# Performance work log

Measured on AMD Instinct MI355X. Metric: run time of the kernel, lower is better.

Reference implementation:

```python
import jax, jax.numpy as jnp
import numpy as np

CONF_THRES = 0.1
IOU_THRES = 0.6
MAX_DET = 300
MAX_WH = 4096.0  # class offset for non-agnostic NMS
NEG_SLOPE = 0.01  # nn.LeakyReLU default


def xywh2xyxy(p):
    xy, wh = p[..., :2], p[..., 2:4]
    return jnp.concatenate([xy - wh / 2, xy + wh / 2], axis=-1)


def pairwise_iou(a, b):
    area_a = (a[:, 2] - a[:, 0]) * (a[:, 3] - a[:, 1])
    area_b = (b[:, 2] - b[:, 0]) * (b[:, 3] - b[:, 1])
    lt = jnp.maximum(a[:, None, :2], b[None, :, :2])
    rb = jnp.minimum(a[:, None, 2:], b[None, :, 2:])
    wh = jnp.clip(rb - lt, 0.0)
    inter = wh[..., 0] * wh[..., 1]
    return inter / (area_a[:, None] + area_b[None, :] - inter + 1e-7)


def nms_single(pred):  # pred: [N, 5+nc]
    boxes = xywh2xyxy(pred[:, :4])
    scores = pred[:, 5:] * pred[:, 4:5]  # obj * cls
    conf = jnp.max(scores, axis=1)
    cls = jnp.argmax(scores, axis=1)
    conf = jnp.where(conf > CONF_THRES, conf, 0.0)
    topv, topi = jax.lax.top_k(conf, MAX_DET)
    b = boxes[topi]                      # [K,4]
    c = cls[topi]
    valid = topv > CONF_THRES
    bo = b + (c.astype(b.dtype) * MAX_WH)[:, None]  # class-offset boxes
    iou = pairwise_iou(bo, bo)           # [K,K]
    idx = jnp.arange(MAX_DET)
    def body(i, keep):
        sup = keep[i] & (iou[i] > IOU_THRES) & (idx > i)
        return keep & ~sup
    keep = jax.lax.fori_loop(0, MAX_DET, body, valid)
    return b, keep


def bilinear_sample(feat, y, x):  # feat [C,H,W], y/x [K,P] -> [C,K,P]
    C, H, W = feat.shape
    y = jnp.clip(y, 0.0, H - 1.0)
    x = jnp.clip(x, 0.0, W - 1.0)
    y0 = jnp.floor(y).astype(jnp.int32)
    x0 = jnp.floor(x).astype(jnp.int32)
    y1 = jnp.minimum(y0 + 1, H - 1)
    x1 = jnp.minimum(x0 + 1, W - 1)
    ly = y - y0
    lx = x - x0
    return (feat[:, y0, x0] * ((1 - ly) * (1 - lx))
            + feat[:, y0, x1] * ((1 - ly) * lx)
            + feat[:, y1, x0] * (ly * (1 - lx))
            + feat[:, y1, x1] * (ly * lx))


def roi_align_1x1(feat, boxes, scale):  # feat [C,H,W], boxes [K,4] xyxy (input-px)
    b = boxes * scale
    w = jnp.maximum(b[:, 2] - b[:, 0], 1.0)
    h = jnp.maximum(b[:, 3] - b[:, 1], 1.0)
    off = jnp.array([0.5, 1.5], dtype=boxes.dtype)
    xs = b[:, 0:1] + off[None, :] * (w[:, None] / 2.0)  # [K,2]
    ys = b[:, 1:2] + off[None, :] * (h[:, None] / 2.0)
    yy = ys[:, jnp.array([0, 0, 1, 1])]  # [K,4] 2x2 grid
    xx = xs[:, jnp.array([0, 1, 0, 1])]
    v = bilinear_sample(feat, yy, xx)    # [C,K,4]
    return jnp.mean(v, axis=2).T         # [K,C]


def rescale_boxes(bbox, hw, hw0):  # scale_coords + normalize by orig shape
    gain = jnp.minimum(hw[0] / hw0[0], hw[1] / hw0[1])
    pad_x = (hw[1] - hw0[1] * gain) / 2.0
    pad_y = (hw[0] - hw0[0] * gain) / 2.0
    x1 = jnp.clip((bbox[:, 0] - pad_x) / gain, 0.0, hw0[1])
    y1 = jnp.clip((bbox[:, 1] - pad_y) / gain, 0.0, hw0[0])
    x2 = jnp.clip((bbox[:, 2] - pad_x) / gain, 0.0, hw0[1])
    y2 = jnp.clip((bbox[:, 3] - pad_y) / gain, 0.0, hw0[0])
    # divide by shapes[i][0] indexed [w,h,w,h]
    return jnp.stack([x1 / hw0[1], y1 / hw0[0], x2 / hw0[1], y2 / hw0[0]], axis=1)


def setup_inputs() -> dict:
    key = jax.random.key(0)
    ks = jax.random.split(key, 10)
    B, N, NC = 8, 25500, 80
    xy = jax.random.uniform(ks[0], (B, N, 2), minval=0.0, maxval=640.0)
    wh = jax.random.uniform(ks[1], (B, N, 2), minval=8.0, maxval=160.0)
    obj = jax.random.uniform(ks[2], (B, N, 1))
    cls = jax.random.uniform(ks[3], (B, N, NC))
    preds = jnp.concatenate([xy, wh, obj, cls], axis=-1)
    feat1 = jax.random.normal(ks[4], (B, 128, 80, 80), dtype=jnp.float32)
    feat2 = jax.random.normal(ks[5], (B, 256, 40, 40), dtype=jnp.float32)
    feat3 = jax.random.normal(ks[6], (B, 512, 20, 20), dtype=jnp.float32)
    feat4 = jax.random.normal(ks[7], (B, 1024, 10, 10), dtype=jnp.float32)
    orig_hw = jnp.tile(jnp.array([[720.0, 1280.0]], dtype=jnp.float32), (B, 1))
    W1 = jax.random.normal(ks[8], (1920, 256), dtype=jnp.float32) * 0.02
    b1 = jnp.zeros((256,), dtype=jnp.float32)
    W2 = jax.random.normal(ks[9], (256, 256), dtype=jnp.float32) * 0.02
    b2 = jnp.zeros((256,), dtype=jnp.float32)
    return {"preds": preds, "feat1": feat1, "feat2": feat2, "feat3": feat3,
            "feat4": feat4, "orig_hw": orig_hw, "W1": W1, "b1": b1,
            "W2": W2, "b2": b2}


def reference(preds, feat1, feat2, feat3, feat4, orig_hw, W1, b1, W2, b2):
    preds = jax.lax.stop_gradient(preds)  # out.detach() in the original
    hw = jnp.array(feat1.shape[-2:], dtype=preds.dtype) * 8.0  # network input h,w
    boxes, keep = jax.vmap(nms_single)(preds)  # [B,K,4], [B,K]
    f1 = jax.vmap(lambda f, b: roi_align_1x1(f, b, 1.0 / 8))(feat1, boxes)
    f2 = jax.vmap(lambda f, b: roi_align_1x1(f, b, 1.0 / 16))(feat2, boxes)
    f3 = jax.vmap(lambda f, b: roi_align_1x1(f, b, 1.0 / 32))(feat3, boxes)
    f4 = jax.vmap(lambda f, b: roi_align_1x1(f, b, 1.0 / 64))(feat4, boxes)
    f = jnp.concatenate([f1, f2, f3, f4], axis=-1)  # [B,K,1920]
    h = jax.nn.leaky_relu(f @ W1 + b1, NEG_SLOPE)
    h = jax.nn.leaky_relu(h @ W2 + b2, NEG_SLOPE)   # [B,K,256]
    bb = jax.vmap(lambda b, s: rescale_boxes(b, hw, s))(boxes, orig_hw)
    out = jnp.concatenate([bb, h], axis=-1)  # [B,K,260]
    return out * keep[..., None].astype(out.dtype)
```

## Files before the change

### kernel.cpp

```cpp
#include <hip/hip_runtime.h>
#include <hip/hip_bf16.h>
#include <cstdint>
#include <cstddef>

#define NBATCH 8
#define NANCH 25500
#define MAXDET 300
#define NBINS 2048
#define SCAT_BLKS 64

typedef __bf16 bf16x8 __attribute__((ext_vector_type(8)));
typedef float floatx4 __attribute__((ext_vector_type(4)));
typedef unsigned long long ull;

__device__ __forceinline__ int conf_bin(float v) {
  unsigned bits = __float_as_uint(v);
  int bin = (int)((bits - 0x3D800000u) >> 14);
  return bin > (NBINS - 1) ? (NBINS - 1) : bin;
}

#define CONF_TILE 64
__global__ __launch_bounds__(256) void conf_kernel(const float* __restrict__ preds,
                                                   float* __restrict__ conf,
                                                   int* __restrict__ cls,
                                                   int* __restrict__ ghist, int total) {
  __shared__ float s[CONF_TILE * 85];
  int base = blockIdx.x * CONF_TILE;
  int nA = total - base; if (nA > CONF_TILE) nA = CONF_TILE;
  int n4 = (nA * 85) >> 2;
  const float4* g4 = (const float4*)(preds + (size_t)base * 85);
  float4* s4 = (float4*)s;
  for (int i = threadIdx.x; i < n4; i += 256) s4[i] = g4[i];
  __syncthreads();
  int lane16 = threadIdx.x & 15;
  int sub = threadIdx.x >> 4;
  #pragma unroll
  for (int r = 0; r < 4; ++r) {
    int a = r * 16 + sub;
    if (a < nA) {
      const float* row = s + a * 85;
      float obj = row[4];
      float best = -1.0f; int bc = 0;
      #pragma unroll
      for (int j = 0; j < 5; ++j) {
        int c = lane16 * 5 + j;
        float v = row[5 + c] * obj;
        if (v > best) { best = v; bc = c; }
      }
      #pragma unroll
      for (int m = 1; m < 16; m <<= 1) {
        float ov = __shfl_xor(best, m, 64);
        int   oc = __shfl_xor(bc,   m, 64);
        if (ov > best || (ov == best && oc < bc)) { best = ov; bc = oc; }
      }
      if (lane16 == 0) {
        int idx = base + a;
        bool pass = best > 0.1f;
        conf[idx] = pass ? best : 0.0f;
        cls[idx] = bc;
        if (pass) {
          int b = idx / NANCH;
          atomicAdd(&ghist[b * NBINS + conf_bin(best)], 1);
        }
      }
    }
  }
}

struct TransArgs {
  const float* src[6];
  __hip_bfloat16* dst[6];
  int C[6], HW[6], tx[6], tpb[6], start[6];
};

__global__ __launch_bounds__(256) void trans_scatter_kernel(TransArgs a,
                                                            const float* __restrict__ conf,
                                                            const float* __restrict__ preds,
                                                            const int* __restrict__ clsg,
                                                            const int* __restrict__ ghist,
                                                            int* __restrict__ gcnt,
                                                            float* __restrict__ gV,
                                                            int* __restrict__ gI,
                                                            float4* __restrict__ gBox) {
  #pragma clang fp contract(off)
  __shared__ __align__(16) char smem[8448];
  int bid = blockIdx.x;
  int t = threadIdx.y * 32 + threadIdx.x;

  if (bid < SCAT_BLKS) {
    int b = bid >> 3, seg = bid & 7;
    int* s_suf = (int*)smem;
    int* shv   = (int*)(smem + 8192);
    int r[8], suf[8], rs[8];
    int w = t >> 6, lane = t & 63;
    if (t == 0) shv[0] = NBINS;
    {
      #pragma unroll
      for (int k = 0; k < 8; ++k)
        r[k] = ghist[b * NBINS + (w * 8 + k) * 64 + lane];
      int bsum = 0;
      #pragma unroll
      for (int k = 0; k < 8; ++k) {
        int s = r[k];
        #pragma unroll
        for (int d = 1; d < 64; d <<= 1) {
          int o = __shfl_down(s, d, 64);
          if (lane + d < 64) s += o;
        }
        suf[k] = s - r[k];
        rs[k] = __shfl(s, 0, 64);
        bsum += rs[k];
      }
      if (lane == 0) shv[4 + w] = bsum;
    }
    __syncthreads();
    {
      int p1 = shv[5], p2 = shv[6], p3 = shv[7];
      int total = shv[4] + p1 + p2 + p3;
      int target = total < 300 ? total : 300;
      int RS = (w == 0) ? (p1 + p2 + p3) : (w == 1) ? (p2 + p3) : (w == 2) ? p3 : 0;
      int run = RS;
      #pragma unroll
      for (int k = 7; k >= 0; --k) {
        int Sx = run + suf[k] + r[k];
        int Sx1 = Sx - r[k];
        int bin = (w * 8 + k) * 64 + lane;
        s_suf[bin] = Sx1;
        if (total > 0 && Sx >= target && Sx1 < target) shv[0] = bin;
        run += rs[k];
      }
    }
    __syncthreads();
    int T = shv[0];
    const int N4 = NANCH >> 2;
    int i0 = (N4 * seg) >> 3, i1 = (N4 * (seg + 1)) >> 3;
    const float4* cf4 = (const float4*)(conf + (size_t)b * NANCH);
    for (int i = i0 + t; i < i1; i += 256) {
      float4 v4 = cf4[i];
      int ib = i * 4;
      float vv[4] = {v4.x, v4.y, v4.z, v4.w};
      #pragma unroll
      for (int q = 0; q < 4; ++q) {
        float v = vv[q];
        if (v > 0.1f) {
          int bin = conf_bin(v);
          if (bin >= T) {
            int slot = s_suf[bin] + atomicAdd(&gcnt[b * NBINS + bin], 1);
            int idx = ib + q;
            const float* p = preds + ((size_t)b * NANCH + idx) * 85;
            float cx = p[0], cy = p[1], wq = p[2], hq = p[3];
            float hw2 = wq * 0.5f, hh2 = hq * 0.5f;
            float x1 = cx - hw2, y1 = cy - hh2, x2 = cx + hw2, y2 = cy + hh2;
            int c = clsg[(size_t)b * NANCH + idx];
            size_t g = (size_t)b * NANCH + slot;
            gV[g] = v;
            gI[g] = idx | (c << 20);
            gBox[g] = make_float4(x1, y1, x2, y2);
          }
        }
      }
    }
    return;
  }

  {
    float (*tile)[33] = (float(*)[33])smem;
    int bid2 = bid - SCAT_BLKS;
    int s = 0;
    #pragma unroll
    for (int i = 1; i < 6; ++i) if (bid2 >= a.start[i]) s = i;
    int local = bid2 - a.start[s];
    int C = a.C[s], HW = a.HW[s], tx0 = a.tx[s], tpb = a.tpb[s];
    int b = local / tpb;
    int rem = local - b * tpb;
    int p0 = (rem % tx0) * 32;
    int c0 = (rem / tx0) * 32;
    const float* inb = a.src[s] + (size_t)b * C * HW;
    __hip_bfloat16* outb = a.dst[s] + (size_t)b * C * HW;
    int tx = threadIdx.x, ty = threadIdx.y;
    #pragma unroll
    for (int k = 0; k < 32; k += 8) {
      int c = c0 + ty + k, p = p0 + tx;
      if (c < C && p < HW) tile[ty + k][tx] = inb[(size_t)c * HW + p];
    }
    __syncthreads();
    #pragma unroll
    for (int k = 0; k < 32; k += 8) {
      int p = p0 + ty + k, c = c0 + tx;
      if (p < HW && c < C) outb[(size_t)p * C + c] = __float2bfloat16(tile[tx][ty + k]);
    }
  }
}

__global__ __launch_bounds__(1024) void nms_kernel(const float* __restrict__ gV,
                                                   const int* __restrict__ gI,
                                                   const float4* __restrict__ gBox,
                                                   const int* __restrict__ ghist,
                                                   float* __restrict__ boxesWs, int* __restrict__ keepWs,
                                                   const float* __restrict__ orig_hw,
                                                   float* __restrict__ out) {
  #pragma clang fp contract(off)
  __shared__ __align__(16) char smem[30208];
  int*    s_h  = (int*)smem;
  float4* bo4  = (float4*)(smem + 8192);
  float (*bxx)[4] = (float(*)[4])(smem + 12992);
  ull   (*mask)[5] = (ull(*)[5])(smem + 17792);
  ull* keepw = (ull*)(smem + 29792);
  ull* nzrow = (ull*)(smem + 29832);
  int* shv   = (int*)(smem + 29872);
  int b = blockIdx.x;
  int t = threadIdx.x;

  if (t < 300) {
    bo4[t] = make_float4(0.0f, 0.0f, 0.0f, 0.0f);
    bxx[t][0] = 0.0f; bxx[t][1] = 0.0f; bxx[t][2] = 0.0f; bxx[t][3] = 0.0f;
  }
  if (t < 5) nzrow[t] = 0ULL;
  if (t == 0) { shv[0] = NBINS; shv[2] = 0; }
  {
    int r[8], suf[8], rs[8];
    int w = t >> 6, lane = t & 63;
    if (t < 256) {
      #pragma unroll
      for (int k = 0; k < 8; ++k)
        r[k] = ghist[b * NBINS + (w * 8 + k) * 64 + lane];
      int bsum = 0;
      #pragma unroll
      for (int k = 0; k < 8; ++k) {
        int s = r[k];
        #pragma unroll
        for (int d = 1; d < 64; d <<= 1) {
          int o = __shfl_down(s, d, 64);
          if (lane + d < 64) s += o;
        }
        suf[k] = s - r[k];
        rs[k] = __shfl(s, 0, 64);
        bsum += rs[k];
      }
      if (lane == 0) shv[4 + w] = bsum;
    }
    __syncthreads();
    if (t < 256) {
      int p1 = shv[5], p2 = shv[6], p3 = shv[7];
      int total = shv[4] + p1 + p2 + p3;
      int target = total < 300 ? total : 300;
      int RS = (w == 0) ? (p1 + p2 + p3) : (w == 1) ? (p2 + p3) : (w == 2) ? p3 : 0;
      int run = RS;
      #pragma unroll
      for (int k = 7; k >= 0; --k) {
        int Sx = run + suf[k] + r[k];
        int Sx1 = Sx - r[k];
        int bin = (w * 8 + k) * 64 + lane;
        s_h[bin] = Sx;
        if (total > 0 && Sx >= target && Sx1 < target) { shv[0] = bin; shv[2] = Sx; }
        run += rs[k];
      }
      if (t == 0) shv[1] = total;
    }
  }
  __syncthreads();
  int total = shv[1];
  int Kslots = shv[2];
  int nvalid = total < 300 ? total : 300;

  if (t >= nvalid && t < 300) {
    size_t bi = ((size_t)(b * 300 + t)) * 4;
    boxesWs[bi + 0] = 0.0f; boxesWs[bi + 1] = 0.0f;
    boxesWs[bi + 2] = 0.0f; boxesWs[bi + 3] = 0.0f;
  }
  if (t < 5) {
    int n = nvalid - t * 64;
    keepw[t] = (n <= 0) ? 0ULL : (n >= 64 ? ~0ULL : ((1ULL << n) - 1ULL));
  }

  {
    const float* vb = gV + (size_t)b * NANCH;
    const int*   ib2 = gI + (size_t)b * NANCH;
    for (int sIdx = t; sIdx < Kslots; sIdx += 1024) {
      float v = vb[sIdx];
      unsigned code = (unsigned)ib2[sIdx];
      int id = (int)(code & 0xFFFFFu);
      int bin = conf_bin(v);
      int lo = (bin + 1 < NBINS) ? s_h[bin + 1] : 0;
      int hi = s_h[bin];
      int rank = lo;
      for (int j = lo; j < hi; ++j) {
        float vj = vb[j];
        int ij = ib2[j] & 0xFFFFF;
        int gt = vj > v;
        int eq = (vj == v) & (ij < id);
        rank += gt | eq;
      }
      if (rank < 300) {
        float4 bx = gBox[(size_t)b * NANCH + sIdx];
        bxx[rank][0] = bx.x; bxx[rank][1] = bx.y; bxx[rank][2] = bx.z; bxx[rank][3] = bx.w;
        size_t bi = ((size_t)(b * 300 + rank)) * 4;
        boxesWs[bi + 0] = bx.x; boxesWs[bi + 1] = bx.y;
        boxesWs[bi + 2] = bx.z; boxesWs[bi + 3] = bx.w;
        int c = (int)(code >> 20);
        float off = (float)c * 4096.0f;
        float4 ob; ob.x = bx.x + off; ob.y = bx.y + off; ob.z = bx.z + off; ob.w = bx.w + off;
        bo4[rank] = ob;
      }
    }
  }
  __syncthreads();

  {
    int wv2 = t >> 6, ln = t & 63;
    if (wv2 < 10) {
      int w2 = wv2 >> 1, half = wv2 & 1;
      int j = w2 * 64 + ln;
      int jc = j < 300 ? j : 0;
      float4 jb = bo4[jc];
      float ja = (jb.z - jb.x) * (jb.w - jb.y);
      bool jv = j < 300;
      int iend = w2 * 64 + 64; if (iend > 300) iend = 300;
      int i0 = half * 150, i1 = i0 + 150; if (i1 > iend) i1 = iend;
      #pragma unroll 4
      for (int i = i0; i < i1; ++i) {
        float4 ib = bo4[i];
        float ai = (ib.z - ib.x) * (ib.w - ib.y);
        float ltx = fmaxf(ib.x, jb.x);
        float lty = fmaxf(ib.y, jb.y);
        float rbx = fminf(ib.z, jb.z);
        float rby = fminf(ib.w, jb.w);
        float wx = fmaxf(rbx - ltx, 0.0f);
        float wy = fmaxf(rby - lty, 0.0f);
        float inter = wx * wy;
        float iou = inter / (ai + ja - inter + 1e-7f);
        ull bal = __ballot(jv && (j > i) && (iou > 0.6f));
        if (ln == 0) {
          mask[i][w2] = bal;
          if (bal) atomicOr(&nzrow[i >> 6], 1ULL << (i & 63));
        }
      }
    }
  }
  __syncthreads();
  if (t == 0) {
    ull kw[5], nz[5];
    #pragma unroll
    for (int w2 = 0; w2 < 5; ++w2) { kw[w2] = keepw[w2]; nz[w2] = nzrow[w2]; }
    #pragma unroll
    for (int w2 = 0; w2 < 5; ++w2) {
      ull p = kw[w2] & nz[w2];
      while (p) {
        int l2 = __builtin_ctzll(p);
        p &= p - 1;
        int i = w2 * 64 + l2;
        for (int w3 = w2; w3 < 5; ++w3) {
          ull m = mask[i][w3];
          kw[w3] &= ~m;
          if (w3 == w2) p &= ~m;
        }
      }
    }
    #pragma unroll
    for (int w2 = 0; w2 < 5; ++w2) keepw[w2] = kw[w2];
  }
  __syncthreads();
  if (t < 300) {
    int kp = (int)((keepw[t >> 6] >> (t & 63)) & 1ULL);
    keepWs[b * 300 + t] = kp;
    float oh = orig_hw[b * 2 + 0], ow = orig_hw[b * 2 + 1];
    float gain = fminf(640.0f / oh, 640.0f / ow);
    float padx = (640.0f - ow * gain) * 0.5f;
    float pady = (640.0f - oh * gain) * 0.5f;
    float x1 = fminf(fmaxf((bxx[t][0] - padx) / gain, 0.0f), ow) / ow;
    float y1 = fminf(fmaxf((bxx[t][1] - pady) / gain, 0.0f), oh) / oh;
    float x2 = fminf(fmaxf((bxx[t][2] - padx) / gain, 0.0f), ow) / ow;
    float y2 = fminf(fmaxf((bxx[t][3] - pady) / gain, 0.0f), oh) / oh;
    size_t o = ((size_t)(b * 300 + t)) * 260;
    out[o + 0] = kp ? x1 : 0.0f;
    out[o + 1] = kp ? y1 : 0.0f;
    out[o + 2] = kp ? x2 : 0.0f;
    out[o + 3] = kp ? y2 : 0.0f;
  }
}

__global__ __launch_bounds__(256) void roi_kernel(const float* __restrict__ boxes,
                                                  const __hip_bfloat16* __restrict__ fT1, const __hip_bfloat16* __restrict__ fT2,
                                                  const __hip_bfloat16* __restrict__ fT3, const __hip_bfloat16* __restrict__ fT4,
                                                  __hip_bfloat16* __restrict__ f) {
  int b = blockIdx.x & 7;
  int r = blockIdx.x >> 3;
  __shared__ int t_off[4][16];
  __shared__ float t_w[4][16];
  int t = threadIdx.x;
  const int Hs[4] = {80, 40, 20, 10};
  const int Cs[4] = {128, 256, 512, 1024};
  const float ss[4] = {0.125f, 0.0625f, 0.03125f, 0.015625f};
  size_t bbase = ((size_t)(b * 300 + r)) * 4;
  float bx0 = boxes[bbase + 0];
  float by0 = boxes[bbase + 1];
  float bx1 = boxes[bbase + 2];
  float by1 = boxes[bbase + 3];
  if (t < 64) {
    int lv = t >> 4, k = t & 15, pp = k >> 2, nb = k & 3;
    float s = ss[lv];
    int H = Hs[lv], W = Hs[lv], C = Cs[lv];
    float b0 = bx0 * s, b1 = by0 * s, b2 = bx1 * s, b3 = by1 * s;
    float w = fmaxf(b2 - b0, 1.0f), h = fmaxf(b3 - b1, 1.0f);
    const float offv[2] = {0.5f, 1.5f};
    float px = b0 + offv[pp & 1] * (w * 0.5f);
    float py = b1 + offv[pp >> 1] * (h * 0.5f);
    float y = fminf(fmaxf(py, 0.0f), (float)(H - 1));
    float x = fminf(fmaxf(px, 0.0f), (float)(W - 1));
    int y0 = (int)floorf(y), x0 = (int)floorf(x);
    int y1 = min(y0 + 1, H - 1), x1 = min(x0 + 1, W - 1);
    float ly = y - (float)y0, lx = x - (float)x0;
    int yy = (nb & 2) ? y1 : y0;
    int xx = (nb & 1) ? x1 : x0;
    float wy = (nb & 2) ? ly : (1.0f - ly);
    float wx = (nb & 1) ? lx : (1.0f - lx);
    t_off[lv][k] = (yy * W + xx) * C;
    t_w[lv][k] = wy * wx;
  }
  __syncthreads();
  const __hip_bfloat16* bases[4] = {
    fT1 + (size_t)b * 6400 * 128,
    fT2 + (size_t)b * 1600 * 256,
    fT3 + (size_t)b * 400 * 512,
    fT4 + (size_t)b * 100 * 1024
  };
  __hip_bfloat16* frow = f + (size_t)(b * 300 + r) * 1920;
  int cbase = 0;
  #pragma unroll
  for (int lv = 0; lv < 4; ++lv) {
    int C = Cs[lv];
    const __hip_bfloat16* base = bases[lv];
    for (int c = t; c < C; c += 256) {
      float acc = 0.0f;
      #pragma unroll
      for (int k = 0; k < 16; ++k)
        acc += t_w[lv][k] * __bfloat162float(base[t_off[lv][k] + c]);
      frow[cbase + c] = __float2bfloat16(acc * 0.25f);
    }
    cbase += C;
  }
}

#define GLDS16(gp, lp) __builtin_amdgcn_global_load_lds( \
    (const __attribute__((address_space(1))) unsigned int*)(gp), \
    (__attribute__((address_space(3))) unsigned int*)(lp), 16, 0, 0)

__global__ __launch_bounds__(256) void gemm_tile_kernel(const __hip_bfloat16* __restrict__ A,
                                                        const __hip_bfloat16* __restrict__ BT,
                                                        const float* __restrict__ bias,
                                                        __hip_bfloat16* __restrict__ Cb,
                                                        float* __restrict__ Cf,
                                                        const int* __restrict__ keep,
                                                        int M, int N, int K, int ldc, int coff) {
  __shared__ __hip_bfloat16 sA[2][64 * 64];
  __shared__ __hip_bfloat16 sB[2][64 * 64];
  int tid = threadIdx.x;
  int bm = blockIdx.x * 64, bn = blockIdx.y * 64;
  int wave = tid >> 6, lane = tid & 63;
  int wr = wave >> 1, wc = wave & 1;
  int idx16 = lane & 15, kb = lane >> 4;
  floatx4 acc[2][2] = {};
  int nt = K >> 6;

  auto stage = [&](int buf, int t) {
    int k0 = t << 6;
    #pragma unroll
    for (int i = 0; i < 2; ++i) {
      int c = tid + i * 256;
      int row = c >> 3, cc = c & 7;
      int scc = cc ^ (row & 7);
      GLDS16(A + (size_t)(bm + row) * K + k0 + scc * 8,
             (char*)&sA[buf][0] + c * 16);
    }
    #pragma unroll
    for (int i = 0; i < 2; ++i) {
      int c = tid + i * 256;
      int row = c >> 3, cc = c & 7;
      int scc = cc ^ (row & 7);
      GLDS16(BT + (size_t)(bn + row) * K + k0 + scc * 8,
             (char*)&sB[buf][0] + c * 16);
    }
  };

  stage(0, 0);
  asm volatile("s_waitcnt vmcnt(0)" ::: "memory");
  __syncthreads();
  int cur = 0;
  for (int t = 0; t < nt; ++t) {
    if (t + 1 < nt) stage(cur ^ 1, t + 1);
    const char* Ab = (const char*)&sA[cur][0];
    const char* Bb = (const char*)&sB[cur][0];
    #pragma unroll
    for (int s = 0; s < 2; ++s) {
      bf16x8 af[2], bg[2];
      #pragma unroll
      for (int m = 0; m < 2; ++m) {
        int row = wr * 32 + m * 16 + idx16;
        int chunk = s * 4 + kb;
        af[m] = *(const bf16x8*)(Ab + row * 128 + ((chunk ^ (row & 7)) * 16));
      }
      #pragma unroll
      for (int n = 0; n < 2; ++n) {
        int row = wc * 32 + n * 16 + idx16;
        int chunk = s * 4 + kb;
        bg[n] = *(const bf16x8*)(Bb + row * 128 + ((chunk ^ (row & 7)) * 16));
      }
      #pragma unroll
      for (int m = 0; m < 2; ++m)
        #pragma unroll
        for (int n = 0; n < 2; ++n)
          acc[m][n] = __builtin_amdgcn_mfma_f32_16x16x32_bf16(af[m], bg[n], acc[m][n], 0, 0, 0);
    }
    asm volatile("s_waitcnt vmcnt(0)" ::: "memory");
    __syncthreads();
    cur ^= 1;
  }
  int col = lane & 15, rb4 = (lane >> 4) * 4;
  #pragma unroll
  for (int m = 0; m < 2; ++m) {
    #pragma unroll
    for (int n = 0; n < 2; ++n) {
      #pragma unroll
      for (int r = 0; r < 4; ++r) {
        int orow = bm + wr * 32 + m * 16 + rb4 + r;
        int ocol = bn + wc * 32 + n * 16 + col;
        if (orow >= M) continue;
        float v = acc[m][n][r] + bias[ocol];
        v = (v >= 0.0f) ? v : 0.01f * v;
        if (Cb) Cb[(size_t)orow * N + ocol] = __float2bfloat16(v);
        if (Cf) {
          float km = keep ? (keep[orow] ? 1.0f : 0.0f) : 1.0f;
          Cf[(size_t)orow * ldc + coff + ocol] = v * km;
        }
      }
    }
  }
}

extern "C" void kernel_launch(void* const* d_in, const int* in_sizes, int n_in,
                              void* d_out, int out_size, void* d_ws, size_t ws_size,
                              hipStream_t stream) {
  (void)in_sizes; (void)n_in; (void)out_size; (void)ws_size;
  const float* preds  = (const float*)d_in[0];
  const float* feat1  = (const float*)d_in[1];
  const float* feat2  = (const float*)d_in[2];
  const float* feat3  = (const float*)d_in[3];
  const float* feat4  = (const float*)d_in[4];
  const float* orighw = (const float*)d_in[5];
  const float* W1     = (const float*)d_in[6];
  const float* b1     = (const float*)d_in[7];
  const float* W2     = (const float*)d_in[8];
  const float* b2     = (const float*)d_in[9];
  float* out = (float*)d_out;

  char* ws = (char*)d_ws;
  size_t off = 0;
  auto alloc = [&](size_t bytes) -> void* {
    void* p = ws + off;
    off = (off + bytes + 255) & ~(size_t)255;
    return p;
  };
  const int BN = NBATCH * NANCH;
  float*  conf   = (float*)alloc((size_t)BN * 4);
  int*    cls    = (int*)  alloc((size_t)BN * 4);
  float*  gV     = (float*)alloc((size_t)BN * 4);
  int*    gI     = (int*)  alloc((size_t)BN * 4);
  float4* gBox   = (float4*)alloc((size_t)BN * 16);
  int*    ghist  = (int*)  alloc((size_t)NBATCH * NBINS * 4);
  int*    gcnt   = (int*)  alloc((size_t)NBATCH * NBINS * 4);
  float*  boxes  = (float*)alloc((size_t)NBATCH * 300 * 4 * 4);
  int*    keep   = (int*)  alloc((size_t)NBATCH * 300 * 4);
  __hip_bfloat16* fT1  = (__hip_bfloat16*)alloc((size_t)NBATCH * 6400 * 128 * 2);
  __hip_bfloat16* fT2  = (__hip_bfloat16*)alloc((size_t)NBATCH * 1600 * 256 * 2);
  __hip_bfloat16* fT3  = (__hip_bfloat16*)alloc((size_t)NBATCH * 400 * 512 * 2);
  __hip_bfloat16* fT4  = (__hip_bfloat16*)alloc((size_t)NBATCH * 100 * 1024 * 2);
  __hip_bfloat16* fmat = (__hip_bfloat16*)alloc((size_t)2400 * 1920 * 2);
  __hip_bfloat16* h1b  = (__hip_bfloat16*)alloc((size_t)2400 * 256 * 2);
  __hip_bfloat16* W1T  = (__hip_bfloat16*)alloc((size_t)256 * 1920 * 2);
  __hip_bfloat16* W2T  = (__hip_bfloat16*)alloc((size_t)256 * 256 * 2);

  hipMemsetAsync(ghist, 0, (size_t)NBATCH * NBINS * 4 * 2, stream);

  conf_kernel<<<(BN + CONF_TILE - 1) / CONF_TILE, 256, 0, stream>>>(preds, conf, cls, ghist, BN);

  TransArgs ta;
  ta.src[0] = feat1; ta.dst[0] = fT1; ta.C[0] = 128;  ta.HW[0] = 6400; ta.tx[0] = 200;
  ta.src[1] = feat2; ta.dst[1] = fT2; ta.C[1] = 256;  ta.HW[1] = 1600; ta.tx[1] = 50;
  ta.src[2] = feat3; ta.dst[2] = fT3; ta.C[2] = 512;  ta.HW[2] = 400;  ta.tx[2] = 13;
  ta.src[3] = feat4; ta.dst[3] = fT4; ta.C[3] = 1024; ta.HW[3] = 100;  ta.tx[3] = 4;
  ta.src[4] = W1;    ta.dst[4] = W1T; ta.C[4] = 1920; ta.HW[4] = 256;  ta.tx[4] = 8;
  ta.src[5] = W2;    ta.dst[5] = W2T; ta.C[5] = 256;  ta.HW[5] = 256;  ta.tx[5] = 8;
  int n_tiles = 0;
  for (int s = 0; s < 6; ++s) {
    int ty = (ta.C[s] + 31) / 32;
    int nbatch = (s < 4) ? NBATCH : 1;
    ta.tpb[s] = ta.tx[s] * ty;
    ta.start[s] = n_tiles;
    n_tiles += ta.tpb[s] * nbatch;
  }
  trans_scatter_kernel<<<SCAT_BLKS + n_tiles, dim3(32, 8), 0, stream>>>(ta, conf, preds, cls,
                                                                        ghist, gcnt,
                                                                        gV, gI, gBox);

  nms_kernel<<<NBATCH, 1024, 0, stream>>>(gV, gI, gBox, ghist, boxes, keep, orighw, out);

  roi_kernel<<<2400, 256, 0, stream>>>(boxes, fT1, fT2, fT3, fT4, fmat);
  gemm_tile_kernel<<<dim3(38, 4), 256, 0, stream>>>(fmat, W1T, b1, h1b, nullptr, nullptr,
                                                    2400, 256, 1920, 0, 0);
  gemm_tile_kernel<<<dim3(38, 4), 256, 0, stream>>>(h1b, W2T, b2, nullptr, out, keep,
                                                    2400, 256, 256, 260, 4);
}
```

Measured before the change: 145.2 us.

## Move confidence histogram into scatter kernel and fold memset into conf kernel

Removes the global per-anchor atomic histogram from conf_kernel; the 64 scatter blocks now build per-segment histograms in shared memory, merge them into the global histogram, and wait on a per-batch spin counter before computing the threshold. The separate hipMemsetAsync is replaced by zeroing in the first blocks of conf_kernel. This cuts global atomic contention and one launch, but adds an inter-block spin barrier that relies on all 8 segment blocks of a batch being co-resident, plus an extra pass over conf.

```diff
diff --git a/kernel.cpp b/kernel.cpp
--- a/kernel.cpp
+++ b/kernel.cpp
@@ -23,7 +23,16 @@
 __global__ __launch_bounds__(256) void conf_kernel(const float* __restrict__ preds,
                                                    float* __restrict__ conf,
                                                    int* __restrict__ cls,
-                                                   int* __restrict__ ghist, int total) {
+                                                   int* __restrict__ zmem, int zints,
+                                                   int total) {
+  if (blockIdx.x < 33) {
+    int base = blockIdx.x * 1024;
+    #pragma unroll
+    for (int k = 0; k < 4; ++k) {
+      int i = base + k * 256 + threadIdx.x;
+      if (i < zints) zmem[i] = 0;
+    }
+  }
   __shared__ float s[CONF_TILE * 85];
   int base = blockIdx.x * CONF_TILE;
   int nA = total - base; if (nA > CONF_TILE) nA = CONF_TILE;
@@ -55,13 +64,8 @@
       }
       if (lane16 == 0) {
         int idx = base + a;
-        bool pass = best > 0.1f;
-        conf[idx] = pass ? best : 0.0f;
+        conf[idx] = (best > 0.1f) ? best : 0.0f;
         cls[idx] = bc;
-        if (pass) {
-          int b = idx / NANCH;
-          atomicAdd(&ghist[b * NBINS + conf_bin(best)], 1);
-        }
       }
     }
   }
@@ -77,8 +81,9 @@
                                                             const float* __restrict__ conf,
                                                             const float* __restrict__ preds,
                                                             const int* __restrict__ clsg,
-                                                            const int* __restrict__ ghist,
+                                                            int* __restrict__ ghist,
                                                             int* __restrict__ gcnt,
+                                                            int* __restrict__ ctr1,
                                                             float* __restrict__ gV,
                                                             int* __restrict__ gI,
                                                             float4* __restrict__ gBox) {
@@ -89,15 +94,43 @@
 
   if (bid < SCAT_BLKS) {
     int b = bid >> 3, seg = bid & 7;
-    int* s_suf = (int*)smem;
-    int* shv   = (int*)(smem + 8192);
+    int* s_h = (int*)smem;
+    int* shv = (int*)(smem + 8192);
+    #pragma unroll
+    for (int k = 0; k < 8; ++k) s_h[t + k * 256] = 0;
+    if (t == 0) shv[0] = NBINS;
+    __syncthreads();
+    const int N4 = NANCH >> 2;
+    int i0 = (N4 * seg) >> 3, i1 = (N4 * (seg + 1)) >> 3;
+    const float4* cf4 = (const float4*)(conf + (size_t)b * NANCH);
+    for (int i = i0 + t; i < i1; i += 256) {
+      float4 v = cf4[i];
+      if (v.x > 0.1f) atomicAdd(&s_h[conf_bin(v.x)], 1);
+      if (v.y > 0.1f) atomicAdd(&s_h[conf_bin(v.y)], 1);
+      if (v.z > 0.1f) atomicAdd(&s_h[conf_bin(v.z)], 1);
+      if (v.w > 0.1f) atomicAdd(&s_h[conf_bin(v.w)], 1);
+    }
+    __syncthreads();
+    #pragma unroll
+    for (int k = 0; k < 8; ++k) {
+      int bin = t + k * 256;
+      int c = s_h[bin];
+      if (c) atomicAdd(&ghist[b * NBINS + bin], c);
+    }
+    __syncthreads();
+    if (t == 0) {
+      __threadfence();
+      atomicAdd(&ctr1[b], 1);
+      while (atomicAdd(&ctr1[b], 0) < 8) __builtin_amdgcn_s_sleep(2);
+      __threadfence();
+    }
+    __syncthreads();
     int r[8], suf[8], rs[8];
     int w = t >> 6, lane = t & 63;
-    if (t == 0) shv[0] = NBINS;
     {
       #pragma unroll
       for (int k = 0; k < 8; ++k)
-        r[k] = ghist[b * NBINS + (w * 8 + k) * 64 + lane];
+        r[k] = atomicAdd(&ghist[b * NBINS + (w * 8 + k) * 64 + lane], 0);
       int bsum = 0;
       #pragma unroll
       for (int k = 0; k < 8; ++k) {
@@ -125,16 +158,13 @@
         int Sx = run + suf[k] + r[k];
         int Sx1 = Sx - r[k];
         int bin = (w * 8 + k) * 64 + lane;
-        s_suf[bin] = Sx1;
+        s_h[bin] = Sx1;
         if (total > 0 && Sx >= target && Sx1 < target) shv[0] = bin;
         run += rs[k];
       }
     }
     __syncthreads();
     int T = shv[0];
-    const int N4 = NANCH >> 2;
-    int i0 = (N4 * seg) >> 3, i1 = (N4 * (seg + 1)) >> 3;
-    const float4* cf4 = (const float4*)(conf + (size_t)b * NANCH);
     for (int i = i0 + t; i < i1; i += 256) {
       float4 v4 = cf4[i];
       int ib = i * 4;
@@ -145,7 +175,7 @@
         if (v > 0.1f) {
           int bin = conf_bin(v);
           if (bin >= T) {
-            int slot = s_suf[bin] + atomicAdd(&gcnt[b * NBINS + bin], 1);
+            int slot = s_h[bin] + atomicAdd(&gcnt[b * NBINS + bin], 1);
             int idx = ib + q;
             const float* p = preds + ((size_t)b * NANCH + idx) * 85;
             float cx = p[0], cy = p[1], wq = p[2], hq = p[3];
@@ -568,6 +598,8 @@
   float4* gBox   = (float4*)alloc((size_t)BN * 16);
   int*    ghist  = (int*)  alloc((size_t)NBATCH * NBINS * 4);
   int*    gcnt   = (int*)  alloc((size_t)NBATCH * NBINS * 4);
+  int*    ctr1   = (int*)  alloc(256);
+  const int zints = NBATCH * NBINS * 2 + 64;
   float*  boxes  = (float*)alloc((size_t)NBATCH * 300 * 4 * 4);
   int*    keep   = (int*)  alloc((size_t)NBATCH * 300 * 4);
   __hip_bfloat16* fT1  = (__hip_bfloat16*)alloc((size_t)NBATCH * 6400 * 128 * 2);
@@ -579,9 +611,8 @@
   __hip_bfloat16* W1T  = (__hip_bfloat16*)alloc((size_t)256 * 1920 * 2);
   __hip_bfloat16* W2T  = (__hip_bfloat16*)alloc((size_t)256 * 256 * 2);
 
-  hipMemsetAsync(ghist, 0, (size_t)NBATCH * NBINS * 4 * 2, stream);
-
-  conf_kernel<<<(BN + CONF_TILE - 1) / CONF_TILE, 256, 0, stream>>>(preds, conf, cls, ghist, BN);
+  conf_kernel<<<(BN + CONF_TILE - 1) / CONF_TILE, 256, 0, stream>>>(preds, conf, cls,
+                                                                    ghist, zints, BN);
 
   TransArgs ta;
   ta.src[0] = feat1; ta.dst[0] = fT1; ta.C[0] = 128;  ta.HW[0] = 6400; ta.tx[0] = 200;
@@ -599,7 +630,7 @@
     n_tiles += ta.tpb[s] * nbatch;
   }
   trans_scatter_kernel<<<SCAT_BLKS + n_tiles, dim3(32, 8), 0, stream>>>(ta, conf, preds, cls,
-                                                                        ghist, gcnt,
+                                                                        ghist, gcnt, ctr1,
                                                                         gV, gI, gBox);
 
   nms_kernel<<<NBATCH, 1024, 0, stream>>>(gV, gI, gBox, ghist, boxes, keep, orighw, out);
```

Result: faster. 133.3 us (-8.2%).
